# Kernel optimization log

Hardware: AMD Instinct MI355X
Metric: run time of the kernel (lower is better)

Reference implementation:

```python
import jax, jax.numpy as jnp
import numpy as np

NFPS = 10

def setup_inputs() -> dict:
    key = jax.random.key(0)
    k1, k2, k3, k4 = jax.random.split(key, 4)
    B, D_IN, H, D_OUT = 131072, 2 * NFPS * 3, 256, NFPS * 3 * 12
    x = jax.random.normal(k1, (B, D_IN), dtype=jnp.float32)
    centres = jax.random.normal(k2, (H, D_IN), dtype=jnp.float32)
    sigmas = jax.random.uniform(k3, (H,), dtype=jnp.float32)
    W2 = jax.random.normal(k4, (D_OUT, H), dtype=jnp.float32) * (1.0 / np.sqrt(H))
    return {"x": x, "centres": centres, "sigmas": sigmas, "W2": W2}

def reference(x, centres, sigmas, W2):
    # RBF layer: distances = ||x - c|| * sigma; gaussian: exp(-distances^2)
    x2 = jnp.sum(x * x, axis=-1, keepdims=True)            # [B,1]
    c2 = jnp.sum(centres * centres, axis=-1)               # [H]
    xc = jnp.einsum('bd,hd->bh', x, centres)               # [B,H]
    d2 = jnp.maximum(x2 + c2[None, :] - 2.0 * xc, 0.0)     # squared distance, clamp fp noise
    phi = jnp.exp(-(sigmas[None, :] ** 2) * d2)            # [B,H]
    out = jnp.einsum('bh,oh->bo', phi, W2)                 # [B, nFPs*3*12]
    B = x.shape[0]
    out = out.reshape(B, NFPS, 12, 3).transpose(0, 1, 3, 2).reshape(B, 3 * NFPS, 12)
    return out
```

## Files before the change

### kernel.cpp

```cpp
#include <hip/hip_runtime.h>

#define THREADS 512
#define DIN 60
#define HN 256
#define DOUT 360

typedef __attribute__((ext_vector_type(8))) short short8;
typedef __attribute__((ext_vector_type(16))) float f32x16;
typedef __attribute__((ext_vector_type(4))) float f32x4;
typedef __attribute__((ext_vector_type(2))) float f32x2;
typedef __attribute__((ext_vector_type(4))) unsigned int u32x4;

#define WS_CBF   0
#define WS_CN    32768
#define WS_W2    34816

__device__ __forceinline__ short bf16_bits(float f) {
    union { float f; unsigned u; } v; v.f = f;
    unsigned r = (v.u + 0x7FFFu + ((v.u >> 16) & 1u)) >> 16;
    return (short)(unsigned short)r;
}

__device__ __forceinline__ unsigned pk_bf16(float a, float b) {
    unsigned r;
    asm("v_cvt_pk_bf16_f32 %0, %1, %2" : "=v"(r) : "v"(a), "v"(b));
    return r;
}

__device__ __forceinline__ void gload16(const void* g, void* lds) {
    __builtin_amdgcn_global_load_lds(
        (const __attribute__((address_space(1))) unsigned int*)(uintptr_t)g,
        (__attribute__((address_space(3))) unsigned int*)(unsigned int)(uintptr_t)lds,
        16, 0, 0);
}

__global__ void prep(const float* __restrict__ centres, const float* __restrict__ sigmas,
                     const float* __restrict__ W2, short* __restrict__ ws)
{
    int t = blockIdx.x * 256 + threadIdx.x;
    if (t < 12288) {
        int row = t >> 5, pc = t & 31;
        int c = pc ^ (row & 31);
        short8 v = {0,0,0,0,0,0,0,0};
        if (row < DOUT) {
            int rr = row / 12, jj = row % 12;
            int fcl = rr / 3, kk = rr % 3;
            int o = fcl * 36 + jj * 3 + kk;
            const float* src = W2 + o * HN + c * 8;
            #pragma unroll
            for (int i = 0; i < 8; ++i) v[i] = bf16_bits(src[i]);
        }
        *(short8*)(ws + (WS_W2 / 2) + t * 8) = v;
    } else if (t < 14336) {
        int j = t - 12288;
        int row = j >> 3, p = j & 7;
        int c = p ^ (row & 7);
        short8 v = {0,0,0,0,0,0,0,0};
        const float* cr = centres + row * DIN;
        if (c < 7) {
            #pragma unroll
            for (int i = 0; i < 8; ++i) {
                int k = c * 8 + i;
                if (k < DIN) v[i] = bf16_bits(cr[k]);
            }
        } else {
            #pragma unroll
            for (int i = 0; i < 4; ++i) v[i] = bf16_bits(cr[56 + i]);
            float c2 = 0.f;
            #pragma unroll
            for (int d = 0; d < DIN; ++d) c2 = fmaf(cr[d], cr[d], c2);
            union { unsigned u; float f; } hb;
            hb.u = ((unsigned)(unsigned short)bf16_bits(c2)) << 16;
            float c2lo = c2 - hb.f;
            v[4] = bf16_bits(-0.5f * hb.f);
            v[5] = bf16_bits(-0.5f * c2lo);
            v[6] = bf16_bits(-0.5f);
            v[7] = bf16_bits(-0.5f);
        }
        *(short8*)(ws + (WS_CBF / 2) + j * 8) = v;
    } else if (t < 14592) {
        int i = t - 14336;
        float sg = sigmas[i];
        ((float*)ws)[WS_CN / 4 + i] = 2.f * sg * sg * 1.44269504088896340736f;
    }
}

__device__ __forceinline__ void load_xtile(const float* __restrict__ x, int row0,
                                           int l31, int hi, short8 xb[4]) {
    const float* xr = x + (size_t)(row0 + l31) * DIN;
    f32x4 xa[4][2];
    #pragma unroll
    for (int kt = 0; kt < 4; ++kt) {
        int k0 = kt * 16 + hi * 8;
        xa[kt][0] = *(const f32x4*)(xr + k0);
        xa[kt][1] = (k0 + 4 < DIN) ? *(const f32x4*)(xr + k0 + 4) : (f32x4){0.f,0.f,0.f,0.f};
    }
    float p2 = 0.f;
    #pragma unroll
    for (int kt = 0; kt < 4; ++kt)
        #pragma unroll
        for (int h = 0; h < 2; ++h)
            #pragma unroll
            for (int i = 0; i < 4; ++i) p2 = fmaf(xa[kt][h][i], xa[kt][h][i], p2);
    float x2v = p2 + __shfl_xor(p2, 32);
    union { unsigned u; float f; } hb; hb.u = pk_bf16(x2v, 0.f) << 16;
    float x2lo = x2v - hb.f;
    #pragma unroll
    for (int kt = 0; kt < 4; ++kt) {
        union { u32x4 u; short8 s; } a;
        a.u[0] = pk_bf16(xa[kt][0][0], xa[kt][0][1]);
        a.u[1] = pk_bf16(xa[kt][0][2], xa[kt][0][3]);
        a.u[2] = pk_bf16(xa[kt][1][0], xa[kt][1][1]);
        a.u[3] = pk_bf16(xa[kt][1][2], xa[kt][1][3]);
        if (kt == 3) {
            a.u[2] = hi ? 0x3F803F80u : a.u[2];
            a.u[3] = hi ? pk_bf16(hb.f, x2lo) : a.u[3];
        }
        xb[kt] = a.s;
    }
}

__global__ __launch_bounds__(THREADS, 2)
void rbf_main(const float* __restrict__ x, const short* __restrict__ ws,
              float* __restrict__ out)
{
    __shared__ short8 w2h[6144];
    __shared__ short8 cbf[2048];
    __shared__ __attribute__((aligned(16))) float nsl[HN];

    const int tid  = threadIdx.x;
    const int w    = tid >> 6;
    const int lane = tid & 63;
    const int l31  = lane & 31;
    const int hi   = lane >> 5;
    const int bid  = blockIdx.x;
    const int f     = (bid >> 3) & 1;
    const int sbase = (bid & 7) | ((bid >> 4) << 3);

    #pragma unroll
    for (int i = 0; i < 12; ++i)
        gload16(ws + (WS_W2 / 2) + ((size_t)f * 6144 + i * THREADS + tid) * 8,
                (char*)w2h + (i * THREADS + tid) * 16);
    #pragma unroll
    for (int i = 0; i < 4; ++i)
        gload16(ws + (WS_CBF / 2) + (i * THREADS + tid) * 8, (char*)cbf + (i * THREADS + tid) * 16);
    if (tid < 64)
        gload16(ws + (WS_CN / 2) + tid * 8, (char*)nsl + tid * 16);

    __syncthreads();

    for (int pit = 0; pit < 2; ++pit) {
        const int rb = sbase * 1024 + pit * 512 + w * 64;

        short8 xb0[4], xb1[4];
        load_xtile(x, rb,      l31, hi, xb0);
        load_xtile(x, rb + 32, l31, hi, xb1);

        unsigned pw0[32][2], pw1[32][2];
        #pragma unroll
        for (int h2 = 0; h2 < 2; ++h2) {
            f32x16 a0[4], a1v[4];
            #pragma unroll
            for (int nt = 0; nt < 4; ++nt) { a0[nt] = (f32x16){}; a1v[nt] = (f32x16){}; }
            __builtin_amdgcn_s_setprio(1);
            #pragma unroll
            for (int nt = 0; nt < 4; ++nt) {
                int row = (h2 * 4 + nt) * 32 + l31;
                #pragma unroll
                for (int kt = 0; kt < 4; ++kt) {
                    short8 cf = cbf[row * 8 + ((kt * 2 + hi) ^ (row & 7))];
                    a0[nt]  = __builtin_amdgcn_mfma_f32_32x32x16_bf16(cf, xb0[kt], a0[nt], 0, 0, 0);
                    a1v[nt] = __builtin_amdgcn_mfma_f32_32x32x16_bf16(cf, xb1[kt], a1v[nt], 0, 0, 0);
                }
            }
            __builtin_amdgcn_s_setprio(0);
            #pragma unroll
            for (int nt = 0; nt < 4; ++nt) {
                int ntg = h2 * 4 + nt;
                #pragma unroll
                for (int q = 0; q < 4; ++q) {
                    f32x4 ns4 = *(const f32x4*)(nsl + ntg * 32 + 8 * q + 4 * hi);
                    float p0[4], p1[4];
                    #pragma unroll
                    for (int j = 0; j < 4; ++j) {
                        p0[j] = exp2f(fminf(ns4[j] * a0[nt][4 * q + j],  0.f));
                        p1[j] = exp2f(fminf(ns4[j] * a1v[nt][4 * q + j], 0.f));
                    }
                    pw0[ntg * 4 + q][0] = pk_bf16(p0[0], p0[1]);
                    pw0[ntg * 4 + q][1] = pk_bf16(p0[2], p0[3]);
                    pw1[ntg * 4 + q][0] = pk_bf16(p1[0], p1[1]);
                    pw1[ntg * 4 + q][1] = pk_bf16(p1[2], p1[3]);
                }
            }
        }

        #pragma unroll
        for (int pass = 0; pass < 2; ++pass) {
            f32x16 c0[3], c1[3];
            #pragma unroll
            for (int nt = 0; nt < 3; ++nt) { c0[nt] = (f32x16){}; c1[nt] = (f32x16){}; }

            #pragma unroll
            for (int kt = 0; kt < 16; ++kt) {
                unsigned d00 = pw0[2 * kt][0], s00 = pw0[2 * kt + 1][0];
                unsigned d01 = pw0[2 * kt][1], s01 = pw0[2 * kt + 1][1];
                asm("v_permlane32_swap_b32 %0, %1" : "+v"(d00), "+v"(s00));
                asm("v_permlane32_swap_b32 %0, %1" : "+v"(d01), "+v"(s01));
                unsigned d10 = pw1[2 * kt][0], s10 = pw1[2 * kt + 1][0];
                unsigned d11 = pw1[2 * kt][1], s11 = pw1[2 * kt + 1][1];
                asm("v_permlane32_swap_b32 %0, %1" : "+v"(d10), "+v"(s10));
                asm("v_permlane32_swap_b32 %0, %1" : "+v"(d11), "+v"(s11));
                union { u32x4 u; short8 s; } b0, b1;
                b0.u[0] = d00; b0.u[1] = d01; b0.u[2] = s00; b0.u[3] = s01;
                b1.u[0] = d10; b1.u[1] = d11; b1.u[2] = s10; b1.u[3] = s11;

                __builtin_amdgcn_s_setprio(1);
                #pragma unroll
                for (int nt = 0; nt < 3; ++nt) {
                    int lrow = (pass * 3 + nt) * 32 + l31;
                    short8 wf = w2h[lrow * 32 + ((kt * 2 + hi) ^ l31)];
                    c0[nt] = __builtin_amdgcn_mfma_f32_32x32x16_bf16(wf, b0.s, c0[nt], 0, 0, 0);
                    c1[nt] = __builtin_amdgcn_mfma_f32_32x32x16_bf16(wf, b1.s, c1[nt], 0, 0, 0);
                }
                __builtin_amdgcn_s_setprio(0);
            }

            #pragma unroll
            for (int t = 0; t < 2; ++t) {
                float* op = out + (size_t)(rb + t * 32 + l31) * DOUT + f * 192 + pass * 96;
                #pragma unroll
                for (int nt = 0; nt < 3; ++nt) {
                    const f32x16& cc = t ? c1[nt] : c0[nt];
                    #pragma unroll
                    for (int q = 0; q < 4; ++q) {
                        int col = f * 192 + pass * 96 + nt * 32 + q * 8 + hi * 4;
                        if (col < DOUT) {
                            f32x4 v;
                            v[0] = cc[4 * q + 0]; v[1] = cc[4 * q + 1];
                            v[2] = cc[4 * q + 2]; v[3] = cc[4 * q + 3];
                            *(f32x4*)(op + nt * 32 + q * 8 + hi * 4) = v;
                        }
                    }
                }
            }
        }
    }
}

extern "C" void kernel_launch(void* const* d_in, const int* in_sizes, int n_in,
                              void* d_out, int out_size, void* d_ws, size_t ws_size,
                              hipStream_t stream) {
    const float* x       = (const float*)d_in[0];
    const float* centres = (const float*)d_in[1];
    const float* sigmas  = (const float*)d_in[2];
    const float* W2      = (const float*)d_in[3];
    float* out = (float*)d_out;
    short* ws  = (short*)d_ws;
    prep<<<dim3(57), dim3(256), 0, stream>>>(centres, sigmas, W2, ws);
    rbf_main<<<dim3(256), dim3(THREADS), 0, stream>>>(x, ws, out);
}
```

Measured before the change: 66.73 us.

## Fuse weight preprocessing into main kernel and prefetch first x tile before barrier

Removes the separate prep kernel and workspace. Each block now converts W2 and the centres to bf16 in its swizzled LDS layout, and computes the scaled sigma table, directly from the fp32 inputs. This removes one kernel launch and the dependency gap between the two kernels. The cost is that every block repeats the conversion work and reads the fp32 weights (roughly twice the bytes of the bf16 copy). The first x tile load is also hoisted above the barrier so it overlaps the LDS fill.

```diff
diff --git a/kernel.cpp b/kernel.cpp
--- a/kernel.cpp
+++ b/kernel.cpp
@@ -11,78 +11,10 @@
 typedef __attribute__((ext_vector_type(2))) float f32x2;
 typedef __attribute__((ext_vector_type(4))) unsigned int u32x4;
 
-#define WS_CBF   0
-#define WS_CN    32768
-#define WS_W2    34816
-
-__device__ __forceinline__ short bf16_bits(float f) {
-    union { float f; unsigned u; } v; v.f = f;
-    unsigned r = (v.u + 0x7FFFu + ((v.u >> 16) & 1u)) >> 16;
-    return (short)(unsigned short)r;
-}
-
 __device__ __forceinline__ unsigned pk_bf16(float a, float b) {
     unsigned r;
     asm("v_cvt_pk_bf16_f32 %0, %1, %2" : "=v"(r) : "v"(a), "v"(b));
     return r;
-}
-
-__device__ __forceinline__ void gload16(const void* g, void* lds) {
-    __builtin_amdgcn_global_load_lds(
-        (const __attribute__((address_space(1))) unsigned int*)(uintptr_t)g,
-        (__attribute__((address_space(3))) unsigned int*)(unsigned int)(uintptr_t)lds,
-        16, 0, 0);
-}
-
-__global__ void prep(const float* __restrict__ centres, const float* __restrict__ sigmas,
-                     const float* __restrict__ W2, short* __restrict__ ws)
-{
-    int t = blockIdx.x * 256 + threadIdx.x;
-    if (t < 12288) {
-        int row = t >> 5, pc = t & 31;
-        int c = pc ^ (row & 31);
-        short8 v = {0,0,0,0,0,0,0,0};
-        if (row < DOUT) {
-            int rr = row / 12, jj = row % 12;
-            int fcl = rr / 3, kk = rr % 3;
-            int o = fcl * 36 + jj * 3 + kk;
-            const float* src = W2 + o * HN + c * 8;
-            #pragma unroll
-            for (int i = 0; i < 8; ++i) v[i] = bf16_bits(src[i]);
-        }
-        *(short8*)(ws + (WS_W2 / 2) + t * 8) = v;
-    } else if (t < 14336) {
-        int j = t - 12288;
-        int row = j >> 3, p = j & 7;
-        int c = p ^ (row & 7);
-        short8 v = {0,0,0,0,0,0,0,0};
-        const float* cr = centres + row * DIN;
-        if (c < 7) {
-            #pragma unroll
-            for (int i = 0; i < 8; ++i) {
-                int k = c * 8 + i;
-                if (k < DIN) v[i] = bf16_bits(cr[k]);
-            }
-        } else {
-            #pragma unroll
-            for (int i = 0; i < 4; ++i) v[i] = bf16_bits(cr[56 + i]);
-            float c2 = 0.f;
-            #pragma unroll
-            for (int d = 0; d < DIN; ++d) c2 = fmaf(cr[d], cr[d], c2);
-            union { unsigned u; float f; } hb;
-            hb.u = ((unsigned)(unsigned short)bf16_bits(c2)) << 16;
-            float c2lo = c2 - hb.f;
-            v[4] = bf16_bits(-0.5f * hb.f);
-            v[5] = bf16_bits(-0.5f * c2lo);
-            v[6] = bf16_bits(-0.5f);
-            v[7] = bf16_bits(-0.5f);
-        }
-        *(short8*)(ws + (WS_CBF / 2) + j * 8) = v;
-    } else if (t < 14592) {
-        int i = t - 14336;
-        float sg = sigmas[i];
-        ((float*)ws)[WS_CN / 4 + i] = 2.f * sg * sg * 1.44269504088896340736f;
-    }
 }
 
 __device__ __forceinline__ void load_xtile(const float* __restrict__ x, int row0,
@@ -121,7 +53,8 @@
 }
 
 __global__ __launch_bounds__(THREADS, 2)
-void rbf_main(const float* __restrict__ x, const short* __restrict__ ws,
+void rbf_main(const float* __restrict__ x, const float* __restrict__ centres,
+              const float* __restrict__ sigmas, const float* __restrict__ W2,
               float* __restrict__ out)
 {
     __shared__ short8 w2h[6144];
@@ -138,23 +71,69 @@
     const int sbase = (bid & 7) | ((bid >> 4) << 3);
 
     #pragma unroll
-    for (int i = 0; i < 12; ++i)
-        gload16(ws + (WS_W2 / 2) + ((size_t)f * 6144 + i * THREADS + tid) * 8,
-                (char*)w2h + (i * THREADS + tid) * 16);
-    #pragma unroll
-    for (int i = 0; i < 4; ++i)
-        gload16(ws + (WS_CBF / 2) + (i * THREADS + tid) * 8, (char*)cbf + (i * THREADS + tid) * 16);
-    if (tid < 64)
-        gload16(ws + (WS_CN / 2) + tid * 8, (char*)nsl + tid * 16);
+    for (int i = 0; i < 12; ++i) {
+        int tsk  = i * THREADS + tid;
+        int lrow = tsk >> 5, pc = tsk & 31;
+        int c    = pc ^ (lrow & 31);
+        int row  = f * 192 + lrow;
+        union { u32x4 u; short8 s; } v; v.u = (u32x4){0u,0u,0u,0u};
+        if (row < DOUT) {
+            int rr = row / 12, jj = row % 12;
+            int fcl = rr / 3, kk = rr % 3;
+            int o = fcl * 36 + jj * 3 + kk;
+            const float* src = W2 + o * HN + c * 8;
+            f32x4 a = *(const f32x4*)src, b = *(const f32x4*)(src + 4);
+            v.u[0] = pk_bf16(a[0], a[1]); v.u[1] = pk_bf16(a[2], a[3]);
+            v.u[2] = pk_bf16(b[0], b[1]); v.u[3] = pk_bf16(b[2], b[3]);
+        }
+        w2h[tsk] = v.s;
+    }
+    #pragma unroll
+    for (int i = 0; i < 4; ++i) {
+        int tsk = i * THREADS + tid;
+        int row = tsk >> 3, p = tsk & 7;
+        int c   = p ^ (row & 7);
+        const float* cr = centres + row * DIN;
+        union { u32x4 u; short8 s; } v;
+        if (c < 7) {
+            f32x4 a = *(const f32x4*)(cr + c * 8), b = *(const f32x4*)(cr + c * 8 + 4);
+            v.u[0] = pk_bf16(a[0], a[1]); v.u[1] = pk_bf16(a[2], a[3]);
+            v.u[2] = pk_bf16(b[0], b[1]); v.u[3] = pk_bf16(b[2], b[3]);
+        } else {
+            f32x4 a = *(const f32x4*)(cr + 56);
+            f32x4 s4 = (f32x4){0.f,0.f,0.f,0.f};
+            #pragma unroll
+            for (int q = 0; q < 15; ++q) {
+                f32x4 t = *(const f32x4*)(cr + 4 * q);
+                s4 += t * t;
+            }
+            float c2 = (s4[0] + s4[1]) + (s4[2] + s4[3]);
+            union { unsigned u; float ff; } hb; hb.u = pk_bf16(c2, 0.f) << 16;
+            float c2lo = c2 - hb.ff;
+            v.u[0] = pk_bf16(a[0], a[1]); v.u[1] = pk_bf16(a[2], a[3]);
+            v.u[2] = pk_bf16(-0.5f * hb.ff, -0.5f * c2lo);
+            v.u[3] = pk_bf16(-0.5f, -0.5f);
+        }
+        cbf[tsk] = v.s;
+    }
+    if (tid < HN) {
+        float sg = sigmas[tid];
+        nsl[tid] = 2.f * sg * sg * 1.44269504088896340736f;
+    }
+
+    const int rb0 = sbase * 1024 + w * 64;
+    short8 xb0[4], xb1[4];
+    load_xtile(x, rb0,      l31, hi, xb0);
+    load_xtile(x, rb0 + 32, l31, hi, xb1);
 
     __syncthreads();
 
     for (int pit = 0; pit < 2; ++pit) {
-        const int rb = sbase * 1024 + pit * 512 + w * 64;
-
-        short8 xb0[4], xb1[4];
-        load_xtile(x, rb,      l31, hi, xb0);
-        load_xtile(x, rb + 32, l31, hi, xb1);
+        const int rb = rb0 + pit * 512;
+        if (pit) {
+            load_xtile(x, rb,      l31, hi, xb0);
+            load_xtile(x, rb + 32, l31, hi, xb1);
+        }
 
         unsigned pw0[32][2], pw1[32][2];
         #pragma unroll
@@ -227,7 +206,7 @@
 
             #pragma unroll
             for (int t = 0; t < 2; ++t) {
-                float* op = out + (size_t)(rb + t * 32 + l31) * DOUT + f * 192 + pass * 96;
+                float* op = out + (size_t)(rb + t * 32 + l31) * DOUT;
                 #pragma unroll
                 for (int nt = 0; nt < 3; ++nt) {
                     const f32x16& cc = t ? c1[nt] : c0[nt];
@@ -238,7 +217,7 @@
                             f32x4 v;
                             v[0] = cc[4 * q + 0]; v[1] = cc[4 * q + 1];
                             v[2] = cc[4 * q + 2]; v[3] = cc[4 * q + 3];
-                            *(f32x4*)(op + nt * 32 + q * 8 + hi * 4) = v;
+                            *(f32x4*)(op + col) = v;
                         }
                     }
                 }
@@ -255,7 +234,5 @@
     const float* sigmas  = (const float*)d_in[2];
     const float* W2      = (const float*)d_in[3];
     float* out = (float*)d_out;
-    short* ws  = (short*)d_ws;
-    prep<<<dim3(57), dim3(256), 0, stream>>>(centres, sigmas, W2, ws);
-    rbf_main<<<dim3(256), dim3(THREADS), 0, stream>>>(x, ws, out);
-}
+    rbf_main<<<dim3(256), dim3(THREADS), 0, stream>>>(x, centres, sigmas, W2, out);
+}
```

Result: slower. 108.0 us (+61.8%).

## Fold sigma scaling into centres and stream per-tile GEMM chain with prefetch

Applied to the files above, without the earlier changes.

Pre-multiplies the bf16 centre table and the norm terms by the per-centre sigma factor in the prep kernel, which drops the per-element scale multiply and the shared sigma table from the main kernel. The main loop now handles one 32-row tile per wave at a time. Each 32-column chunk of the first GEMM goes through exp and straight into the second GEMM, keeping all six output accumulators live. This replaces holding the full phi matrix for two tiles in registers. The next x tile is loaded before the output stores. The intent is lower register pressure and better overlap, at the cost of less MFMA interleaving and some extra bf16 rounding error from the scaled centres.

```diff
diff --git a/kernel.cpp b/kernel.cpp
--- a/kernel.cpp
+++ b/kernel.cpp
@@ -8,12 +8,10 @@
 typedef __attribute__((ext_vector_type(8))) short short8;
 typedef __attribute__((ext_vector_type(16))) float f32x16;
 typedef __attribute__((ext_vector_type(4))) float f32x4;
-typedef __attribute__((ext_vector_type(2))) float f32x2;
 typedef __attribute__((ext_vector_type(4))) unsigned int u32x4;
 
 #define WS_CBF   0
-#define WS_CN    32768
-#define WS_W2    34816
+#define WS_W2    32768
 
 __device__ __forceinline__ short bf16_bits(float f) {
     union { float f; unsigned u; } v; v.f = f;
@@ -55,33 +53,33 @@
         int j = t - 12288;
         int row = j >> 3, p = j & 7;
         int c = p ^ (row & 7);
+        const float* cr = centres + row * DIN;
+        float sg = sigmas[row];
+        union { unsigned u; float f; } nq;
+        nq.u = ((unsigned)(unsigned short)bf16_bits(2.f * sg * sg * 1.44269504088896340736f)) << 16;
+        const float nsq = nq.f;
         short8 v = {0,0,0,0,0,0,0,0};
-        const float* cr = centres + row * DIN;
         if (c < 7) {
             #pragma unroll
             for (int i = 0; i < 8; ++i) {
                 int k = c * 8 + i;
-                if (k < DIN) v[i] = bf16_bits(cr[k]);
+                if (k < DIN) v[i] = bf16_bits(nsq * cr[k]);
             }
         } else {
             #pragma unroll
-            for (int i = 0; i < 4; ++i) v[i] = bf16_bits(cr[56 + i]);
+            for (int i = 0; i < 4; ++i) v[i] = bf16_bits(nsq * cr[56 + i]);
             float c2 = 0.f;
             #pragma unroll
             for (int d = 0; d < DIN; ++d) c2 = fmaf(cr[d], cr[d], c2);
-            union { unsigned u; float f; } hb;
-            hb.u = ((unsigned)(unsigned short)bf16_bits(c2)) << 16;
-            float c2lo = c2 - hb.f;
-            v[4] = bf16_bits(-0.5f * hb.f);
-            v[5] = bf16_bits(-0.5f * c2lo);
-            v[6] = bf16_bits(-0.5f);
-            v[7] = bf16_bits(-0.5f);
+            float T = -0.5f * nsq * c2;
+            union { unsigned u; float f; } th;
+            th.u = ((unsigned)(unsigned short)bf16_bits(T)) << 16;
+            v[4] = bf16_bits(th.f);
+            v[5] = bf16_bits(T - th.f);
+            v[6] = bf16_bits(-0.5f * nsq);
+            v[7] = v[6];
         }
         *(short8*)(ws + (WS_CBF / 2) + j * 8) = v;
-    } else if (t < 14592) {
-        int i = t - 14336;
-        float sg = sigmas[i];
-        ((float*)ws)[WS_CN / 4 + i] = 2.f * sg * sg * 1.44269504088896340736f;
     }
 }
 
@@ -126,7 +124,6 @@
 {
     __shared__ short8 w2h[6144];
     __shared__ short8 cbf[2048];
-    __shared__ __attribute__((aligned(16))) float nsl[HN];
 
     const int tid  = threadIdx.x;
     const int w    = tid >> 6;
@@ -144,102 +141,78 @@
     #pragma unroll
     for (int i = 0; i < 4; ++i)
         gload16(ws + (WS_CBF / 2) + (i * THREADS + tid) * 8, (char*)cbf + (i * THREADS + tid) * 16);
-    if (tid < 64)
-        gload16(ws + (WS_CN / 2) + tid * 8, (char*)nsl + tid * 16);
+
+    short8 xb[4];
+    load_xtile(x, sbase * 1024 + w * 32, l31, hi, xb);
 
     __syncthreads();
 
-    for (int pit = 0; pit < 2; ++pit) {
-        const int rb = sbase * 1024 + pit * 512 + w * 64;
-
-        short8 xb0[4], xb1[4];
-        load_xtile(x, rb,      l31, hi, xb0);
-        load_xtile(x, rb + 32, l31, hi, xb1);
-
-        unsigned pw0[32][2], pw1[32][2];
+    for (int it = 0; it < 4; ++it) {
+        const int rb = sbase * 1024 + it * 256 + w * 32;
+
+        f32x16 acc2[6];
         #pragma unroll
-        for (int h2 = 0; h2 < 2; ++h2) {
-            f32x16 a0[4], a1v[4];
-            #pragma unroll
-            for (int nt = 0; nt < 4; ++nt) { a0[nt] = (f32x16){}; a1v[nt] = (f32x16){}; }
+        for (int nt = 0; nt < 6; ++nt) acc2[nt] = (f32x16){};
+
+        #pragma unroll
+        for (int nt1 = 0; nt1 < 8; ++nt1) {
+            f32x16 a1 = (f32x16){};
+            const int row = nt1 * 32 + l31;
             __builtin_amdgcn_s_setprio(1);
             #pragma unroll
-            for (int nt = 0; nt < 4; ++nt) {
-                int row = (h2 * 4 + nt) * 32 + l31;
+            for (int kt = 0; kt < 4; ++kt) {
+                short8 cf = cbf[row * 8 + ((kt * 2 + hi) ^ (row & 7))];
+                a1 = __builtin_amdgcn_mfma_f32_32x32x16_bf16(cf, xb[kt], a1, 0, 0, 0);
+            }
+            __builtin_amdgcn_s_setprio(0);
+
+            unsigned pwl[4][2];
+            #pragma unroll
+            for (int q = 0; q < 4; ++q) {
+                float ph[4];
                 #pragma unroll
-                for (int kt = 0; kt < 4; ++kt) {
-                    short8 cf = cbf[row * 8 + ((kt * 2 + hi) ^ (row & 7))];
-                    a0[nt]  = __builtin_amdgcn_mfma_f32_32x32x16_bf16(cf, xb0[kt], a0[nt], 0, 0, 0);
-                    a1v[nt] = __builtin_amdgcn_mfma_f32_32x32x16_bf16(cf, xb1[kt], a1v[nt], 0, 0, 0);
+                for (int j = 0; j < 4; ++j)
+                    ph[j] = exp2f(fminf(a1[4 * q + j], 0.f));
+                pwl[q][0] = pk_bf16(ph[0], ph[1]);
+                pwl[q][1] = pk_bf16(ph[2], ph[3]);
+            }
+
+            #pragma unroll
+            for (int m = 0; m < 2; ++m) {
+                unsigned d0 = pwl[2 * m][0], s0 = pwl[2 * m + 1][0];
+                unsigned d1 = pwl[2 * m][1], s1 = pwl[2 * m + 1][1];
+                asm("v_permlane32_swap_b32 %0, %1" : "+v"(d0), "+v"(s0));
+                asm("v_permlane32_swap_b32 %0, %1" : "+v"(d1), "+v"(s1));
+                union { u32x4 u; short8 s; } bfr;
+                bfr.u[0] = d0; bfr.u[1] = d1; bfr.u[2] = s0; bfr.u[3] = s1;
+                const int ktg = nt1 * 2 + m;
+
+                __builtin_amdgcn_s_setprio(1);
+                #pragma unroll
+                for (int nt = 0; nt < 6; ++nt) {
+                    int lrow = nt * 32 + l31;
+                    short8 wf = w2h[lrow * 32 + ((ktg * 2 + hi) ^ l31)];
+                    acc2[nt] = __builtin_amdgcn_mfma_f32_32x32x16_bf16(wf, bfr.s, acc2[nt], 0, 0, 0);
                 }
-            }
-            __builtin_amdgcn_s_setprio(0);
-            #pragma unroll
-            for (int nt = 0; nt < 4; ++nt) {
-                int ntg = h2 * 4 + nt;
+                __builtin_amdgcn_s_setprio(0);
+            }
+        }
+
+        if (it < 3)
+            load_xtile(x, rb + 256, l31, hi, xb);
+
+        {
+            float* op = out + (size_t)(rb + l31) * DOUT;
+            #pragma unroll
+            for (int nt = 0; nt < 6; ++nt) {
                 #pragma unroll
                 for (int q = 0; q < 4; ++q) {
-                    f32x4 ns4 = *(const f32x4*)(nsl + ntg * 32 + 8 * q + 4 * hi);
-                    float p0[4], p1[4];
-                    #pragma unroll
-                    for (int j = 0; j < 4; ++j) {
-                        p0[j] = exp2f(fminf(ns4[j] * a0[nt][4 * q + j],  0.f));
-                        p1[j] = exp2f(fminf(ns4[j] * a1v[nt][4 * q + j], 0.f));
-                    }
-                    pw0[ntg * 4 + q][0] = pk_bf16(p0[0], p0[1]);
-                    pw0[ntg * 4 + q][1] = pk_bf16(p0[2], p0[3]);
-                    pw1[ntg * 4 + q][0] = pk_bf16(p1[0], p1[1]);
-                    pw1[ntg * 4 + q][1] = pk_bf16(p1[2], p1[3]);
-                }
-            }
-        }
-
-        #pragma unroll
-        for (int pass = 0; pass < 2; ++pass) {
-            f32x16 c0[3], c1[3];
-            #pragma unroll
-            for (int nt = 0; nt < 3; ++nt) { c0[nt] = (f32x16){}; c1[nt] = (f32x16){}; }
-
-            #pragma unroll
-            for (int kt = 0; kt < 16; ++kt) {
-                unsigned d00 = pw0[2 * kt][0], s00 = pw0[2 * kt + 1][0];
-                unsigned d01 = pw0[2 * kt][1], s01 = pw0[2 * kt + 1][1];
-                asm("v_permlane32_swap_b32 %0, %1" : "+v"(d00), "+v"(s00));
-                asm("v_permlane32_swap_b32 %0, %1" : "+v"(d01), "+v"(s01));
-                unsigned d10 = pw1[2 * kt][0], s10 = pw1[2 * kt + 1][0];
-                unsigned d11 = pw1[2 * kt][1], s11 = pw1[2 * kt + 1][1];
-                asm("v_permlane32_swap_b32 %0, %1" : "+v"(d10), "+v"(s10));
-                asm("v_permlane32_swap_b32 %0, %1" : "+v"(d11), "+v"(s11));
-                union { u32x4 u; short8 s; } b0, b1;
-                b0.u[0] = d00; b0.u[1] = d01; b0.u[2] = s00; b0.u[3] = s01;
-                b1.u[0] = d10; b1.u[1] = d11; b1.u[2] = s10; b1.u[3] = s11;
-
-                __builtin_amdgcn_s_setprio(1);
-                #pragma unroll
-                for (int nt = 0; nt < 3; ++nt) {
-                    int lrow = (pass * 3 + nt) * 32 + l31;
-                    short8 wf = w2h[lrow * 32 + ((kt * 2 + hi) ^ l31)];
-                    c0[nt] = __builtin_amdgcn_mfma_f32_32x32x16_bf16(wf, b0.s, c0[nt], 0, 0, 0);
-                    c1[nt] = __builtin_amdgcn_mfma_f32_32x32x16_bf16(wf, b1.s, c1[nt], 0, 0, 0);
-                }
-                __builtin_amdgcn_s_setprio(0);
-            }
-
-            #pragma unroll
-            for (int t = 0; t < 2; ++t) {
-                float* op = out + (size_t)(rb + t * 32 + l31) * DOUT + f * 192 + pass * 96;
-                #pragma unroll
-                for (int nt = 0; nt < 3; ++nt) {
-                    const f32x16& cc = t ? c1[nt] : c0[nt];
-                    #pragma unroll
-                    for (int q = 0; q < 4; ++q) {
-                        int col = f * 192 + pass * 96 + nt * 32 + q * 8 + hi * 4;
-                        if (col < DOUT) {
-                            f32x4 v;
-                            v[0] = cc[4 * q + 0]; v[1] = cc[4 * q + 1];
-                            v[2] = cc[4 * q + 2]; v[3] = cc[4 * q + 3];
-                            *(f32x4*)(op + nt * 32 + q * 8 + hi * 4) = v;
-                        }
+                    int col = f * 192 + nt * 32 + q * 8 + hi * 4;
+                    if (col < DOUT) {
+                        f32x4 v;
+                        v[0] = acc2[nt][4 * q + 0]; v[1] = acc2[nt][4 * q + 1];
+                        v[2] = acc2[nt][4 * q + 2]; v[3] = acc2[nt][4 * q + 3];
+                        *(f32x4*)(op + col) = v;
                     }
                 }
             }
@@ -256,6 +229,6 @@
     const float* W2      = (const float*)d_in[3];
     float* out = (float*)d_out;
     short* ws  = (short*)d_ws;
-    prep<<<dim3(57), dim3(256), 0, stream>>>(centres, sigmas, W2, ws);
+    prep<<<dim3(56), dim3(256), 0, stream>>>(centres, sigmas, W2, ws);
     rbf_main<<<dim3(256), dim3(THREADS), 0, stream>>>(x, ws, out);
 }
```

New measurement: 63.12 us. 5.4% less time.
